# Optimization experiments

Measured on AMD Instinct MI355X. Metric: run time of the kernel, lower is better.

The kernel has to match this reference:

```python
import jax, jax.numpy as jnp
import numpy as np

NEG_SLOPE = 0.01  # nn.LeakyReLU default
NUM_GRAPHS = 64


def leaky_relu(x):
    return jnp.where(x >= 0, x, NEG_SLOPE * x)


def gcn_conv(x, edge_index, W, b):
    """PyG GCNConv: add self-loops, symmetric norm, aggregate, + bias."""
    n = x.shape[0]
    h = x @ W  # [N, F]
    loop = jnp.arange(n, dtype=edge_index.dtype)
    src = jnp.concatenate([edge_index[0], loop])
    dst = jnp.concatenate([edge_index[1], loop])
    deg = jax.ops.segment_sum(jnp.ones_like(dst, dtype=h.dtype), dst, num_segments=n)
    dinv = jnp.where(deg > 0, deg ** -0.5, 0.0)
    norm = dinv[src] * dinv[dst]  # [E+N]
    msg = h[src] * norm[:, None]  # [E+N, F] dominant intermediate
    out = jax.ops.segment_sum(msg, dst, num_segments=n)
    return out + b


def gep(x, batch, num_graphs):
    """global mean pool over batch segment ids."""
    s = jax.ops.segment_sum(x, batch, num_segments=num_graphs)
    cnt = jax.ops.segment_sum(jnp.ones(x.shape[0], dtype=x.dtype), batch, num_segments=num_graphs)
    return s / jnp.maximum(cnt, 1.0)[:, None]


def setup_inputs() -> dict:
    key = jax.random.key(0)
    ks = jax.random.split(key, 16)
    N, E, F, D, B = 10000, 80000, 1024, 128, NUM_GRAPHS
    sc = 1.0 / np.sqrt(F)
    inp = {
        "pro1_x": jax.random.normal(ks[0], (N, F), jnp.float32),
        "pro1_edge_index": jax.random.randint(ks[1], (2, E), 0, N, jnp.int64),
        "pro1_batch": jnp.sort(jax.random.randint(ks[2], (N,), 0, B, jnp.int64)),
        "pro2_x": jax.random.normal(ks[3], (N, F), jnp.float32),
        "pro2_edge_index": jax.random.randint(ks[4], (2, E), 0, N, jnp.int64),
        "pro2_batch": jnp.sort(jax.random.randint(ks[5], (N,), 0, B, jnp.int64)),
        "mas1_straight": 0, "mas1_flipped": 0, "mas2_straight": 0, "mas2_flipped": 0,
        "conv1_W": jax.random.normal(ks[6], (F, F), jnp.float32) * sc,
        "conv1_b": jnp.zeros((F,), jnp.float32),
        "fc1_W": jax.random.normal(ks[7], (F, D), jnp.float32) * sc,
        "fc1_b": jnp.zeros((D,), jnp.float32),
        "conv2_W": jax.random.normal(ks[8], (F, F), jnp.float32) * sc,
        "conv2_b": jnp.zeros((F,), jnp.float32),
        "fc2_W": jax.random.normal(ks[9], (F, D), jnp.float32) * sc,
        "fc2_b": jnp.zeros((D,), jnp.float32),
        "final_W": jax.random.normal(ks[10], (2 * D, 1), jnp.float32) * (1.0 / np.sqrt(2 * D)),
        "final_b": jnp.zeros((1,), jnp.float32),
    }
    return inp


def reference(pro1_x, pro1_edge_index, pro1_batch, pro2_x, pro2_edge_index, pro2_batch,
              mas1_straight, mas1_flipped, mas2_straight, mas2_flipped,
              conv1_W, conv1_b, fc1_W, fc1_b, conv2_W, conv2_b, fc2_W, fc2_b,
              final_W, final_b):
    # branch 1 (dropout = identity at inference)
    x = leaky_relu(gcn_conv(pro1_x, pro1_edge_index, conv1_W, conv1_b))
    x = gep(x, pro1_batch, NUM_GRAPHS)
    x = leaky_relu(x @ fc1_W + fc1_b)
    # branch 2
    xt = leaky_relu(gcn_conv(pro2_x, pro2_edge_index, conv2_W, conv2_b))
    xt = gep(xt, pro2_batch, NUM_GRAPHS)
    xt = leaky_relu(xt @ fc2_W + fc2_b)
    combined = jnp.concatenate([x, xt], axis=1)  # [B, 256]
    return combined @ final_W + final_b  # [B, 1]
```

## Files before the change

### kernel.cpp

```cpp
#include <hip/hip_runtime.h>
#include <cstdint>
#include <cstddef>

#define FDIM 1024
#define DDIM 128
#define NGRAPH 64
#define FCH 8
#define QN 4
#define FILLB 320

#define AS1 __attribute__((address_space(1)))
#define AS3 __attribute__((address_space(3)))

typedef float f32x4 __attribute__((ext_vector_type(4)));
typedef short s16x8 __attribute__((ext_vector_type(8)));
typedef unsigned short u16x8 __attribute__((ext_vector_type(8)));

__device__ __forceinline__ unsigned short f2bf(float f) {
  unsigned int x = __float_as_uint(f);
  unsigned int r = (x + 0x7fffu + ((x >> 16) & 1u)) >> 16;
  return (unsigned short)r;
}
__device__ __forceinline__ float bflo(unsigned int v) {
  return __uint_as_float(v << 16);
}
__device__ __forceinline__ float bfhi(unsigned int v) {
  return __uint_as_float(v & 0xffff0000u);
}

__device__ __forceinline__ int lower_bound(const int* a, int n, int v) {
  int lo = 0, hi = n;
  while (lo < hi) {
    int mid = (lo + hi) >> 1;
    if (a[mid] < v) lo = mid + 1; else hi = mid;
  }
  return lo;
}

__global__ __launch_bounds__(256) void k_prep_cast(const int* __restrict__ ei1,
                                                   const int* __restrict__ ei2,
                                                   int* deg1, int* deg2,
                                                   const float4* __restrict__ x1,
                                                   const float4* __restrict__ x2,
                                                   const float* __restrict__ W1,
                                                   const float* __restrict__ W2,
                                                   u16x8* xb1, u16x8* xb2,
                                                   unsigned short* Wt1, unsigned short* Wt2,
                                                   int E, int n8, int gE, int nxb4) {
  __shared__ unsigned short tile[64][65];
  int br = blockIdx.y;
  int x = blockIdx.x, t = threadIdx.x;
  if (x < gE) {
    const int* ei = br ? ei2 : ei1;
    int* deg = br ? deg2 : deg1;
    int i = x * 256 + t;
    if (i < E) atomicAdd(&deg[ei[E + i]], 1);
  } else if (x < gE + nxb4) {
    const float4* xx = br ? x2 : x1;
    u16x8* xb = br ? xb2 : xb1;
    int base = (x - gE) * 1024 + t;
    #pragma unroll
    for (int u = 0; u < 4; ++u) {
      int i = base + u * 256;
      if (i < n8) {
        float4 v0 = xx[2 * i];
        float4 v1 = xx[2 * i + 1];
        u16x8 o;
        o[0] = f2bf(v0.x); o[1] = f2bf(v0.y); o[2] = f2bf(v0.z); o[3] = f2bf(v0.w);
        o[4] = f2bf(v1.x); o[5] = f2bf(v1.y); o[6] = f2bf(v1.z); o[7] = f2bf(v1.w);
        xb[i] = o;
      }
    }
  } else {
    const float* W = br ? W2 : W1;
    unsigned short* Wt = br ? Wt2 : Wt1;
    int tid16 = x - gE - nxb4;
    int kb = tid16 >> 4, nb = tid16 & 15;
    int tn = t & 63, tg = t >> 6;
    #pragma unroll
    for (int r = 0; r < 16; ++r) {
      int kk = tg * 16 + r;
      tile[kk][tn] = f2bf(W[(size_t)(kb * 64 + kk) * FDIM + nb * 64 + tn]);
    }
    __syncthreads();
    #pragma unroll
    for (int r = 0; r < 16; ++r) {
      int nn = tg * 16 + r;
      Wt[(size_t)(nb * 64 + nn) * FDIM + kb * 64 + tn] = tile[tn][nn];
    }
  }
}

#define SCAN_T 1024
#define SCAN_PER 16
__global__ __launch_bounds__(SCAN_T) void k_scan(const int* __restrict__ deg1,
                                                 const int* __restrict__ deg2,
                                                 int* off1, int* off2,
                                                 int* cur1, int* cur2,
                                                 float* dinv1, float* dinv2,
                                                 const int* __restrict__ batch1,
                                                 const int* __restrict__ batch2,
                                                 int* cnt1, int* gstart1,
                                                 int* cnt2, int* gstart2, int n) {
  if (blockIdx.x == 2) {
    int t = threadIdx.x;
    if (t < 128) {
      const int* batch = (t < NGRAPH) ? batch1 : batch2;
      int* cnt = (t < NGRAPH) ? cnt1 : cnt2;
      int* gstart = (t < NGRAPH) ? gstart1 : gstart2;
      int g = t & (NGRAPH - 1);
      int lo = lower_bound(batch, n, g);
      int hi = lower_bound(batch, n, g + 1);
      gstart[g] = lo;
      cnt[g] = hi - lo;
    }
    return;
  }
  const int* deg = blockIdx.x ? deg2 : deg1;
  int* off = blockIdx.x ? off2 : off1;
  int* cur = blockIdx.x ? cur2 : cur1;
  float* dinv = blockIdx.x ? dinv2 : dinv1;
  __shared__ int sums[SCAN_T];
  int t = threadIdx.x;
  int base = t * SCAN_PER;
  int local[SCAN_PER];
  int s = 0;
  #pragma unroll
  for (int i = 0; i < SCAN_PER; ++i) {
    int idx = base + i;
    int d = (idx < n) ? (deg[idx] + 1) : 0;
    local[i] = s;
    s += d;
    if (idx < n) dinv[idx] = rsqrtf((float)d);
  }
  sums[t] = s;
  __syncthreads();
  for (int o = 1; o < SCAN_T; o <<= 1) {
    int v = (t >= o) ? sums[t - o] : 0;
    __syncthreads();
    sums[t] += v;
    __syncthreads();
  }
  int basesum = (t > 0) ? sums[t - 1] : 0;
  #pragma unroll
  for (int i = 0; i < SCAN_PER; ++i) {
    int idx = base + i;
    if (idx < n) { int o = basesum + local[i]; off[idx] = o; cur[idx] = o; }
  }
  if (t == SCAN_T - 1) off[n] = sums[SCAN_T - 1];
}

__global__ __launch_bounds__(256, 3) void k_fill_gemm(const int* __restrict__ ei1,
                                                      const int* __restrict__ ei2,
                                                      int* cur1, int* cur2,
                                                      const float* __restrict__ dinv1,
                                                      const float* __restrict__ dinv2,
                                                      int* adjsrc1, int* adjsrc2,
                                                      float* adjw1, float* adjw2,
                                                      const unsigned short* __restrict__ A1,
                                                      const unsigned short* __restrict__ A2,
                                                      const unsigned short* __restrict__ B1,
                                                      const unsigned short* __restrict__ B2,
                                                      unsigned short* __restrict__ C1,
                                                      unsigned short* __restrict__ C2,
                                                      int E, int N, int M) {
  __shared__ unsigned short sm[24576];
  int br = blockIdx.y;
  if (blockIdx.x < FILLB) {
    const int* ei = br ? ei2 : ei1;
    int* cur = br ? cur2 : cur1;
    const float* dinv = br ? dinv2 : dinv1;
    int* adjsrc = br ? adjsrc2 : adjsrc1;
    float* adjw = br ? adjw2 : adjw1;
    int i = blockIdx.x * 256 + threadIdx.x;
    if (i < E) {
      int s = ei[i];
      int d = ei[E + i];
      int p = atomicAdd(&cur[d], 1);
      adjsrc[p] = s;
      adjw[p] = dinv[s] * dinv[d];
    }
    if (i < N) {
      int p = atomicAdd(&cur[i], 1);
      adjsrc[p] = i;
      adjw[p] = dinv[i] * dinv[i];
    }
    return;
  }
  const unsigned short* A = br ? A2 : A1;
  const unsigned short* Bt = br ? B2 : B1;
  unsigned short* C = br ? C2 : C1;
  const int K = FDIM;
  int tid = threadIdx.x;
  int w = tid >> 6, lane = tid & 63;
  int wm = w >> 1, wn = w & 1;

  int bx = blockIdx.x - FILLB;
  int per_xcd = (gridDim.x - FILLB) >> 3;
  int l = (bx & 7) * per_xcd + (bx >> 3);
  int m0 = (l >> 3) * 128;
  int n0 = (l & 7) * 128;

  int la = lane & 15, u4 = lane >> 4;

  int rs = w * 32 + (lane >> 2);
  int c16 = (lane & 3) ^ ((lane >> 3) & 3);
  const unsigned short* gA0 = A + (size_t)min(m0 + rs, M - 1) * K + c16 * 8;
  const unsigned short* gA1 = A + (size_t)min(m0 + rs + 16, M - 1) * K + c16 * 8;
  const unsigned short* gB0 = Bt + (size_t)(n0 + rs) * K + c16 * 8;
  const unsigned short* gB1 = Bt + (size_t)(n0 + rs + 16) * K + c16 * 8;
  int lbA = w * 1024;

  int sw = ((la >> 1) & 3) ^ u4;
  unsigned raoff = (unsigned)((wm * 64 + la) * 32 + sw * 8);
  unsigned rboff = (unsigned)(4096 + (wn * 64 + la) * 32 + sw * 8);

  f32x4 acc[4][4];
  #pragma unroll
  for (int i = 0; i < 4; ++i)
    #pragma unroll
    for (int j = 0; j < 4; ++j)
      acc[i][j] = (f32x4){0.f, 0.f, 0.f, 0.f};

  auto STAGE = [&](int bb, int kc) {
    int kq = kc * 32;
    int b0 = bb * 8192 + lbA;
    __builtin_amdgcn_global_load_lds((const AS1 unsigned int*)(gA0 + kq),
                                     (AS3 unsigned int*)&sm[b0], 16, 0, 0);
    __builtin_amdgcn_global_load_lds((const AS1 unsigned int*)(gA1 + kq),
                                     (AS3 unsigned int*)&sm[b0 + 512], 16, 0, 0);
    __builtin_amdgcn_global_load_lds((const AS1 unsigned int*)(gB0 + kq),
                                     (AS3 unsigned int*)&sm[b0 + 4096], 16, 0, 0);
    __builtin_amdgcn_global_load_lds((const AS1 unsigned int*)(gB1 + kq),
                                     (AS3 unsigned int*)&sm[b0 + 4096 + 512], 16, 0, 0);
  };

  auto COMPUTE = [&](int bb) {
    const AS3 unsigned short* pa = (const AS3 unsigned short*)&sm[0] + bb * 8192 + raoff;
    const AS3 unsigned short* pb = (const AS3 unsigned short*)&sm[0] + bb * 8192 + rboff;
    s16x8 a0, a1, a2, a3, b0, b1, b2, b3;
    asm volatile("ds_read_b128 %0, %1 offset:0"    : "=v"(a0) : "v"(pa));
    asm volatile("ds_read_b128 %0, %1 offset:1024" : "=v"(a1) : "v"(pa));
    asm volatile("ds_read_b128 %0, %1 offset:2048" : "=v"(a2) : "v"(pa));
    asm volatile("ds_read_b128 %0, %1 offset:3072" : "=v"(a3) : "v"(pa));
    asm volatile("ds_read_b128 %0, %1 offset:0"    : "=v"(b0) : "v"(pb));
    asm volatile("ds_read_b128 %0, %1 offset:1024" : "=v"(b1) : "v"(pb));
    asm volatile("ds_read_b128 %0, %1 offset:2048" : "=v"(b2) : "v"(pb));
    asm volatile("ds_read_b128 %0, %1 offset:3072" : "=v"(b3) : "v"(pb));
    asm volatile("s_waitcnt lgkmcnt(0)" ::: "memory");
    __builtin_amdgcn_sched_barrier(0);
    __builtin_amdgcn_s_setprio(1);
    acc[0][0] = __builtin_amdgcn_mfma_f32_16x16x32_bf16(a0, b0, acc[0][0], 0, 0, 0);
    acc[0][1] = __builtin_amdgcn_mfma_f32_16x16x32_bf16(a0, b1, acc[0][1], 0, 0, 0);
    acc[0][2] = __builtin_amdgcn_mfma_f32_16x16x32_bf16(a0, b2, acc[0][2], 0, 0, 0);
    acc[0][3] = __builtin_amdgcn_mfma_f32_16x16x32_bf16(a0, b3, acc[0][3], 0, 0, 0);
    acc[1][0] = __builtin_amdgcn_mfma_f32_16x16x32_bf16(a1, b0, acc[1][0], 0, 0, 0);
    acc[1][1] = __builtin_amdgcn_mfma_f32_16x16x32_bf16(a1, b1, acc[1][1], 0, 0, 0);
    acc[1][2] = __builtin_amdgcn_mfma_f32_16x16x32_bf16(a1, b2, acc[1][2], 0, 0, 0);
    acc[1][3] = __builtin_amdgcn_mfma_f32_16x16x32_bf16(a1, b3, acc[1][3], 0, 0, 0);
    acc[2][0] = __builtin_amdgcn_mfma_f32_16x16x32_bf16(a2, b0, acc[2][0], 0, 0, 0);
    acc[2][1] = __builtin_amdgcn_mfma_f32_16x16x32_bf16(a2, b1, acc[2][1], 0, 0, 0);
    acc[2][2] = __builtin_amdgcn_mfma_f32_16x16x32_bf16(a2, b2, acc[2][2], 0, 0, 0);
    acc[2][3] = __builtin_amdgcn_mfma_f32_16x16x32_bf16(a2, b3, acc[2][3], 0, 0, 0);
    acc[3][0] = __builtin_amdgcn_mfma_f32_16x16x32_bf16(a3, b0, acc[3][0], 0, 0, 0);
    acc[3][1] = __builtin_amdgcn_mfma_f32_16x16x32_bf16(a3, b1, acc[3][1], 0, 0, 0);
    acc[3][2] = __builtin_amdgcn_mfma_f32_16x16x32_bf16(a3, b2, acc[3][2], 0, 0, 0);
    acc[3][3] = __builtin_amdgcn_mfma_f32_16x16x32_bf16(a3, b3, acc[3][3], 0, 0, 0);
    __builtin_amdgcn_s_setprio(0);
  };

  STAGE(0, 0);
  STAGE(1, 1);
  int sb = 2, cb = 0;
  for (int kt = 0; kt < 30; ++kt) {
    STAGE(sb, kt + 2);
    asm volatile("s_waitcnt vmcnt(8)" ::: "memory");
    __builtin_amdgcn_sched_barrier(0);
    __builtin_amdgcn_s_barrier();
    COMPUTE(cb);
    __builtin_amdgcn_s_barrier();
    sb = (sb == 2) ? 0 : sb + 1;
    cb = (cb == 2) ? 0 : cb + 1;
  }
  asm volatile("s_waitcnt vmcnt(4)" ::: "memory");
  __builtin_amdgcn_sched_barrier(0);
  __builtin_amdgcn_s_barrier();
  COMPUTE(cb);
  __builtin_amdgcn_s_barrier();
  cb = (cb == 2) ? 0 : cb + 1;
  asm volatile("s_waitcnt vmcnt(0)" ::: "memory");
  __builtin_amdgcn_sched_barrier(0);
  __builtin_amdgcn_s_barrier();
  COMPUTE(cb);

  #pragma unroll
  for (int i = 0; i < 4; ++i) {
    int row_base = m0 + wm * 64 + i * 16 + (lane >> 4) * 4;
    #pragma unroll
    for (int j = 0; j < 4; ++j) {
      int col = n0 + wn * 64 + j * 16 + (lane & 15);
      #pragma unroll
      for (int r = 0; r < 4; ++r) {
        int row = row_base + r;
        if (row < M) C[(size_t)row * FDIM + col] = f2bf(acc[i][j][r]);
      }
    }
  }
}

__global__ __launch_bounds__(256) void k_aggpool(const unsigned short* __restrict__ h1,
                                                 const unsigned short* __restrict__ h2,
                                                 const int* __restrict__ off1,
                                                 const int* __restrict__ off2,
                                                 const int* __restrict__ adjsrc1,
                                                 const int* __restrict__ adjsrc2,
                                                 const float* __restrict__ adjw1,
                                                 const float* __restrict__ adjw2,
                                                 const float* __restrict__ bias1,
                                                 const float* __restrict__ bias2,
                                                 const int* __restrict__ cnt1,
                                                 const int* __restrict__ cnt2,
                                                 const int* __restrict__ gstart1,
                                                 const int* __restrict__ gstart2,
                                                 float* pool4_1, float* pool4_2) {
  int br = blockIdx.y;
  const unsigned short* h = br ? h2 : h1;
  const int* off = br ? off2 : off1;
  const int* adjsrc = br ? adjsrc2 : adjsrc1;
  const float* adjw = br ? adjw2 : adjw1;
  const float* bias = br ? bias2 : bias1;
  const int* cnt = br ? cnt2 : cnt1;
  const int* gstart = br ? gstart2 : gstart1;
  float* pool4 = br ? pool4_2 : pool4_1;

  int x = blockIdx.x;
  int chunk = x & (FCH - 1);
  int r = x >> 3;
  int g = r & (NGRAPH - 1);
  int q = r >> 6;

  int t = threadIdx.x;
  int grp = t >> 6, lane = t & 63;

  int n = cnt[g];
  int start = gstart[g];
  int per = (n + QN - 1) / QN;
  int v0 = start + q * per;
  int v1 = min(start + n, v0 + per);

  int colbase = chunk * 128 + lane * 2;
  const unsigned short* hc = h + colbase;
  float2 b2 = *(const float2*)(bias + colbase);
  float s0 = 0.f, s1 = 0.f;

  for (int v = v0 + grp; v < v1; v += 4) {
    int pb = off[v], pe = off[v + 1];
    float a0 = 0.f, a1 = 0.f;
    for (int pbb = pb; pbb < pe; pbb += 64) {
      int m = min(64, pe - pbb);
      int lp = pbb + ((lane < m) ? lane : (m - 1));
      int vs = adjsrc[lp];
      float vw = adjw[lp];
      int j = 0;
      for (; j + 4 <= m; j += 4) {
        int i0 = __shfl(vs, j),     i1 = __shfl(vs, j + 1);
        int i2 = __shfl(vs, j + 2), i3 = __shfl(vs, j + 3);
        float w0 = __shfl(vw, j),     w1 = __shfl(vw, j + 1);
        float w2 = __shfl(vw, j + 2), w3 = __shfl(vw, j + 3);
        unsigned int h0 = *(const unsigned int*)(hc + ((size_t)i0 << 10));
        unsigned int hv1 = *(const unsigned int*)(hc + ((size_t)i1 << 10));
        unsigned int hv2 = *(const unsigned int*)(hc + ((size_t)i2 << 10));
        unsigned int hv3 = *(const unsigned int*)(hc + ((size_t)i3 << 10));
        a0 += w0 * bflo(h0);  a1 += w0 * bfhi(h0);
        a0 += w1 * bflo(hv1); a1 += w1 * bfhi(hv1);
        a0 += w2 * bflo(hv2); a1 += w2 * bfhi(hv2);
        a0 += w3 * bflo(hv3); a1 += w3 * bfhi(hv3);
      }
      for (; j < m; ++j) {
        int i0 = __shfl(vs, j);
        float w0 = __shfl(vw, j);
        unsigned int h0 = *(const unsigned int*)(hc + ((size_t)i0 << 10));
        a0 += w0 * bflo(h0);
        a1 += w0 * bfhi(h0);
      }
    }
    a0 += b2.x; a1 += b2.y;
    s0 += (a0 >= 0.f) ? a0 : 0.01f * a0;
    s1 += (a1 >= 0.f) ? a1 : 0.01f * a1;
  }

  __shared__ float sm[4][128];
  sm[grp][lane * 2] = s0;
  sm[grp][lane * 2 + 1] = s1;
  __syncthreads();
  if (t < 128) {
    float sum = sm[0][t] + sm[1][t] + sm[2][t] + sm[3][t];
    float ic = 1.0f / fmaxf((float)n, 1.0f);
    pool4[((size_t)(q * NGRAPH + g)) * FDIM + chunk * 128 + t] = sum * ic;
  }
}

__global__ __launch_bounds__(256) void k_fc_final(const float* __restrict__ pool4_1,
                                                  const float* __restrict__ pool4_2,
                                                  const float* __restrict__ W1,
                                                  const float* __restrict__ W2,
                                                  const float* __restrict__ b1,
                                                  const float* __restrict__ b2,
                                                  const float* __restrict__ fW,
                                                  const float* __restrict__ fb,
                                                  float* __restrict__ out) {
  int g = blockIdx.x;
  int t = threadIdx.x;
  int half = t >> 7;
  int j = t & 127;
  const float* pool4 = half ? pool4_2 : pool4_1;
  const float* W = half ? W2 : W1;
  const float* b = half ? b2 : b1;
  __shared__ float xs[2][FDIM];
  for (int k = j; k < FDIM; k += DDIM) {
    float v = 0.f;
    #pragma unroll
    for (int q = 0; q < QN; ++q)
      v += pool4[((size_t)(q * NGRAPH + g)) * FDIM + k];
    xs[half][k] = v;
  }
  __syncthreads();
  float a0 = b[j], a1 = 0.f, a2 = 0.f, a3 = 0.f;
  for (int k = 0; k < FDIM; k += 4) {
    a0 += xs[half][k]     * W[(size_t)k * DDIM + j];
    a1 += xs[half][k + 1] * W[(size_t)(k + 1) * DDIM + j];
    a2 += xs[half][k + 2] * W[(size_t)(k + 2) * DDIM + j];
    a3 += xs[half][k + 3] * W[(size_t)(k + 3) * DDIM + j];
  }
  float acc = (a0 + a1) + (a2 + a3);
  acc = (acc >= 0.f) ? acc : 0.01f * acc;
  float c = acc * fW[half * DDIM + j];
  #pragma unroll
  for (int o = 32; o > 0; o >>= 1) c += __shfl_down(c, o);
  __shared__ float ws[4];
  if ((t & 63) == 0) ws[t >> 6] = c;
  __syncthreads();
  if (t == 0) out[g] = ws[0] + ws[1] + ws[2] + ws[3] + fb[0];
}

extern "C" void kernel_launch(void* const* d_in, const int* in_sizes, int n_in,
                              void* d_out, int out_size, void* d_ws, size_t ws_size,
                              hipStream_t stream) {
  const float* x1 = (const float*)d_in[0];
  const int* ei1 = (const int*)d_in[1];
  const int* batch1 = (const int*)d_in[2];
  const float* x2 = (const float*)d_in[3];
  const int* ei2 = (const int*)d_in[4];
  const int* batch2 = (const int*)d_in[5];
  const float* conv1_W = (const float*)d_in[10];
  const float* conv1_b = (const float*)d_in[11];
  const float* fc1_W = (const float*)d_in[12];
  const float* fc1_b = (const float*)d_in[13];
  const float* conv2_W = (const float*)d_in[14];
  const float* conv2_b = (const float*)d_in[15];
  const float* fc2_W = (const float*)d_in[16];
  const float* fc2_b = (const float*)d_in[17];
  const float* final_W = (const float*)d_in[18];
  const float* final_b = (const float*)d_in[19];
  float* out = (float*)d_out;

  const int N = in_sizes[2];
  const int E = in_sizes[1] / 2;
  const int A = E + N;

  size_t off_b = 0;
  auto alloc = [&](size_t bytes) -> void* {
    void* p = (char*)d_ws + off_b;
    off_b += (bytes + 255) & ~(size_t)255;
    return p;
  };
  unsigned short* xbf1 = (unsigned short*)alloc((size_t)N * FDIM * 2);
  unsigned short* xbf2 = (unsigned short*)alloc((size_t)N * FDIM * 2);
  unsigned short* hbf1 = (unsigned short*)alloc((size_t)N * FDIM * 2);
  unsigned short* hbf2 = (unsigned short*)alloc((size_t)N * FDIM * 2);
  unsigned short* Wt1 = (unsigned short*)alloc((size_t)FDIM * FDIM * 2);
  unsigned short* Wt2 = (unsigned short*)alloc((size_t)FDIM * FDIM * 2);
  int* deg1 = (int*)alloc(N * 4);
  int* deg2 = (int*)alloc(N * 4);
  int* cnt1 = (int*)alloc(NGRAPH * 4);
  int* cnt2 = (int*)alloc(NGRAPH * 4);
  int* gstart1 = (int*)alloc(NGRAPH * 4);
  int* gstart2 = (int*)alloc(NGRAPH * 4);
  int* off1 = (int*)alloc((N + 1) * 4);
  int* off2 = (int*)alloc((N + 1) * 4);
  int* cur1 = (int*)alloc(N * 4);
  int* cur2 = (int*)alloc(N * 4);
  float* dinv1 = (float*)alloc(N * 4);
  float* dinv2 = (float*)alloc(N * 4);
  int* adjsrc1 = (int*)alloc((size_t)A * 4);
  int* adjsrc2 = (int*)alloc((size_t)A * 4);
  float* adjw1 = (float*)alloc((size_t)A * 4);
  float* adjw2 = (float*)alloc((size_t)A * 4);
  float* pool4_1 = (float*)alloc((size_t)QN * NGRAPH * FDIM * 4);
  float* pool4_2 = (float*)alloc((size_t)QN * NGRAPH * FDIM * 4);

  const int T = 256;
  int gE = (E + T - 1) / T;
  int n8 = N * FDIM / 8;
  int nxb4 = (n8 + 1023) / 1024;
  int mt = (N + 127) / 128;
  dim3 gPrepCast(gE + nxb4 + 256, 2);
  dim3 gFillGemm(FILLB + mt * 8, 2);
  dim3 gAgg(FCH * NGRAPH * QN, 2);

  size_t degspan = (size_t)((char*)deg2 - (char*)deg1) + (size_t)N * 4;
  hipMemsetAsync(deg1, 0, degspan, stream);
  k_prep_cast<<<gPrepCast, T, 0, stream>>>(ei1, ei2, deg1, deg2,
                                           (const float4*)x1, (const float4*)x2,
                                           conv1_W, conv2_W,
                                           (u16x8*)xbf1, (u16x8*)xbf2, Wt1, Wt2,
                                           E, n8, gE, nxb4);
  k_scan<<<3, SCAN_T, 0, stream>>>(deg1, deg2, off1, off2, cur1, cur2, dinv1, dinv2,
                                   batch1, batch2, cnt1, gstart1, cnt2, gstart2, N);
  k_fill_gemm<<<gFillGemm, T, 0, stream>>>(ei1, ei2, cur1, cur2, dinv1, dinv2,
                                           adjsrc1, adjsrc2, adjw1, adjw2,
                                           xbf1, xbf2, Wt1, Wt2, hbf1, hbf2,
                                           E, N, N);
  k_aggpool<<<gAgg, T, 0, stream>>>(hbf1, hbf2, off1, off2, adjsrc1, adjsrc2,
                                    adjw1, adjw2, conv1_b, conv2_b,
                                    cnt1, cnt2, gstart1, gstart2, pool4_1, pool4_2);
  k_fc_final<<<NGRAPH, T, 0, stream>>>(pool4_1, pool4_2, fc1_W, fc2_W, fc1_b, fc2_b,
                                       final_W, final_b, out);
}
```

Baseline: 318.3 us.

## Process two K-tiles per barrier pair with four-buffer LDS ping-pong in GEMM

```diff
diff --git a/kernel.cpp b/kernel.cpp
--- a/kernel.cpp
+++ b/kernel.cpp
@@ -150,7 +150,7 @@
   if (t == SCAN_T - 1) off[n] = sums[SCAN_T - 1];
 }
 
-__global__ __launch_bounds__(256, 3) void k_fill_gemm(const int* __restrict__ ei1,
+__global__ __launch_bounds__(256, 2) void k_fill_gemm(const int* __restrict__ ei1,
                                                       const int* __restrict__ ei2,
                                                       int* cur1, int* cur2,
                                                       const float* __restrict__ dinv1,
@@ -164,7 +164,7 @@
                                                       unsigned short* __restrict__ C1,
                                                       unsigned short* __restrict__ C2,
                                                       int E, int N, int M) {
-  __shared__ unsigned short sm[24576];
+  __shared__ unsigned short sm[32768];
   int br = blockIdx.y;
   if (blockIdx.x < FILLB) {
     const int* ei = br ? ei2 : ei1;
@@ -235,63 +235,76 @@
                                      (AS3 unsigned int*)&sm[b0 + 4096 + 512], 16, 0, 0);
   };
 
-  auto COMPUTE = [&](int bb) {
-    const AS3 unsigned short* pa = (const AS3 unsigned short*)&sm[0] + bb * 8192 + raoff;
-    const AS3 unsigned short* pb = (const AS3 unsigned short*)&sm[0] + bb * 8192 + rboff;
-    s16x8 a0, a1, a2, a3, b0, b1, b2, b3;
-    asm volatile("ds_read_b128 %0, %1 offset:0"    : "=v"(a0) : "v"(pa));
-    asm volatile("ds_read_b128 %0, %1 offset:1024" : "=v"(a1) : "v"(pa));
-    asm volatile("ds_read_b128 %0, %1 offset:2048" : "=v"(a2) : "v"(pa));
-    asm volatile("ds_read_b128 %0, %1 offset:3072" : "=v"(a3) : "v"(pa));
-    asm volatile("ds_read_b128 %0, %1 offset:0"    : "=v"(b0) : "v"(pb));
-    asm volatile("ds_read_b128 %0, %1 offset:1024" : "=v"(b1) : "v"(pb));
-    asm volatile("ds_read_b128 %0, %1 offset:2048" : "=v"(b2) : "v"(pb));
-    asm volatile("ds_read_b128 %0, %1 offset:3072" : "=v"(b3) : "v"(pb));
+  #define MFMA16(aa, bb)                                                            \
+    acc[0][0] = __builtin_amdgcn_mfma_f32_16x16x32_bf16(aa[0], bb[0], acc[0][0], 0, 0, 0); \
+    acc[0][1] = __builtin_amdgcn_mfma_f32_16x16x32_bf16(aa[0], bb[1], acc[0][1], 0, 0, 0); \
+    acc[0][2] = __builtin_amdgcn_mfma_f32_16x16x32_bf16(aa[0], bb[2], acc[0][2], 0, 0, 0); \
+    acc[0][3] = __builtin_amdgcn_mfma_f32_16x16x32_bf16(aa[0], bb[3], acc[0][3], 0, 0, 0); \
+    acc[1][0] = __builtin_amdgcn_mfma_f32_16x16x32_bf16(aa[1], bb[0], acc[1][0], 0, 0, 0); \
+    acc[1][1] = __builtin_amdgcn_mfma_f32_16x16x32_bf16(aa[1], bb[1], acc[1][1], 0, 0, 0); \
+    acc[1][2] = __builtin_amdgcn_mfma_f32_16x16x32_bf16(aa[1], bb[2], acc[1][2], 0, 0, 0); \
+    acc[1][3] = __builtin_amdgcn_mfma_f32_16x16x32_bf16(aa[1], bb[3], acc[1][3], 0, 0, 0); \
+    acc[2][0] = __builtin_amdgcn_mfma_f32_16x16x32_bf16(aa[2], bb[0], acc[2][0], 0, 0, 0); \
+    acc[2][1] = __builtin_amdgcn_mfma_f32_16x16x32_bf16(aa[2], bb[1], acc[2][1], 0, 0, 0); \
+    acc[2][2] = __builtin_amdgcn_mfma_f32_16x16x32_bf16(aa[2], bb[2], acc[2][2], 0, 0, 0); \
+    acc[2][3] = __builtin_amdgcn_mfma_f32_16x16x32_bf16(aa[2], bb[3], acc[2][3], 0, 0, 0); \
+    acc[3][0] = __builtin_amdgcn_mfma_f32_16x16x32_bf16(aa[3], bb[0], acc[3][0], 0, 0, 0); \
+    acc[3][1] = __builtin_amdgcn_mfma_f32_16x16x32_bf16(aa[3], bb[1], acc[3][1], 0, 0, 0); \
+    acc[3][2] = __builtin_amdgcn_mfma_f32_16x16x32_bf16(aa[3], bb[2], acc[3][2], 0, 0, 0); \
+    acc[3][3] = __builtin_amdgcn_mfma_f32_16x16x32_bf16(aa[3], bb[3], acc[3][3], 0, 0, 0);
+
+  auto COMPUTE_PAIR = [&](int b0i, int b1i) {
+    const AS3 unsigned short* base = (const AS3 unsigned short*)&sm[0];
+    const AS3 unsigned short* pa0 = base + b0i * 8192 + raoff;
+    const AS3 unsigned short* pb0 = base + b0i * 8192 + rboff;
+    const AS3 unsigned short* pa1 = base + b1i * 8192 + raoff;
+    const AS3 unsigned short* pb1 = base + b1i * 8192 + rboff;
+    s16x8 a0[4], b0v[4], a1[4], b1v[4];
+    asm volatile("ds_read_b128 %0, %1 offset:0"    : "=v"(a0[0]) : "v"(pa0));
+    asm volatile("ds_read_b128 %0, %1 offset:1024" : "=v"(a0[1]) : "v"(pa0));
+    asm volatile("ds_read_b128 %0, %1 offset:2048" : "=v"(a0[2]) : "v"(pa0));
+    asm volatile("ds_read_b128 %0, %1 offset:3072" : "=v"(a0[3]) : "v"(pa0));
+    asm volatile("ds_read_b128 %0, %1 offset:0"    : "=v"(b0v[0]) : "v"(pb0));
+    asm volatile("ds_read_b128 %0, %1 offset:1024" : "=v"(b0v[1]) : "v"(pb0));
+    asm volatile("ds_read_b128 %0, %1 offset:2048" : "=v"(b0v[2]) : "v"(pb0));
+    asm volatile("ds_read_b128 %0, %1 offset:3072" : "=v"(b0v[3]) : "v"(pb0));
+    asm volatile("ds_read_b128 %0, %1 offset:0"    : "=v"(a1[0]) : "v"(pa1));
+    asm volatile("ds_read_b128 %0, %1 offset:1024" : "=v"(a1[1]) : "v"(pa1));
+    asm volatile("ds_read_b128 %0, %1 offset:2048" : "=v"(a1[2]) : "v"(pa1));
+    asm volatile("ds_read_b128 %0, %1 offset:3072" : "=v"(a1[3]) : "v"(pa1));
+    asm volatile("ds_read_b128 %0, %1 offset:0"    : "=v"(b1v[0]) : "v"(pb1));
+    asm volatile("ds_read_b128 %0, %1 offset:1024" : "=v"(b1v[1]) : "v"(pb1));
+    asm volatile("ds_read_b128 %0, %1 offset:2048" : "=v"(b1v[2]) : "v"(pb1));
+    asm volatile("ds_read_b128 %0, %1 offset:3072" : "=v"(b1v[3]) : "v"(pb1));
+    asm volatile("s_waitcnt lgkmcnt(8)" ::: "memory");
+    __builtin_amdgcn_sched_barrier(0);
+    __builtin_amdgcn_s_setprio(1);
+    MFMA16(a0, b0v)
+    __builtin_amdgcn_s_setprio(0);
     asm volatile("s_waitcnt lgkmcnt(0)" ::: "memory");
     __builtin_amdgcn_sched_barrier(0);
     __builtin_amdgcn_s_setprio(1);
-    acc[0][0] = __builtin_amdgcn_mfma_f32_16x16x32_bf16(a0, b0, acc[0][0], 0, 0, 0);
-    acc[0][1] = __builtin_amdgcn_mfma_f32_16x16x32_bf16(a0, b1, acc[0][1], 0, 0, 0);
-    acc[0][2] = __builtin_amdgcn_mfma_f32_16x16x32_bf16(a0, b2, acc[0][2], 0, 0, 0);
-    acc[0][3] = __builtin_amdgcn_mfma_f32_16x16x32_bf16(a0, b3, acc[0][3], 0, 0, 0);
-    acc[1][0] = __builtin_amdgcn_mfma_f32_16x16x32_bf16(a1, b0, acc[1][0], 0, 0, 0);
-    acc[1][1] = __builtin_amdgcn_mfma_f32_16x16x32_bf16(a1, b1, acc[1][1], 0, 0, 0);
-    acc[1][2] = __builtin_amdgcn_mfma_f32_16x16x32_bf16(a1, b2, acc[1][2], 0, 0, 0);
-    acc[1][3] = __builtin_amdgcn_mfma_f32_16x16x32_bf16(a1, b3, acc[1][3], 0, 0, 0);
-    acc[2][0] = __builtin_amdgcn_mfma_f32_16x16x32_bf16(a2, b0, acc[2][0], 0, 0, 0);
-    acc[2][1] = __builtin_amdgcn_mfma_f32_16x16x32_bf16(a2, b1, acc[2][1], 0, 0, 0);
-    acc[2][2] = __builtin_amdgcn_mfma_f32_16x16x32_bf16(a2, b2, acc[2][2], 0, 0, 0);
-    acc[2][3] = __builtin_amdgcn_mfma_f32_16x16x32_bf16(a2, b3, acc[2][3], 0, 0, 0);
-    acc[3][0] = __builtin_amdgcn_mfma_f32_16x16x32_bf16(a3, b0, acc[3][0], 0, 0, 0);
-    acc[3][1] = __builtin_amdgcn_mfma_f32_16x16x32_bf16(a3, b1, acc[3][1], 0, 0, 0);
-    acc[3][2] = __builtin_amdgcn_mfma_f32_16x16x32_bf16(a3, b2, acc[3][2], 0, 0, 0);
-    acc[3][3] = __builtin_amdgcn_mfma_f32_16x16x32_bf16(a3, b3, acc[3][3], 0, 0, 0);
+    MFMA16(a1, b1v)
     __builtin_amdgcn_s_setprio(0);
   };
 
   STAGE(0, 0);
   STAGE(1, 1);
-  int sb = 2, cb = 0;
-  for (int kt = 0; kt < 30; ++kt) {
-    STAGE(sb, kt + 2);
+  for (int s = 0; s < 15; ++s) {
+    int pb = ((s + 1) & 1) * 2;
+    STAGE(pb, 2 * s + 2);
+    STAGE(pb + 1, 2 * s + 3);
     asm volatile("s_waitcnt vmcnt(8)" ::: "memory");
     __builtin_amdgcn_sched_barrier(0);
     __builtin_amdgcn_s_barrier();
-    COMPUTE(cb);
+    int cbp = (s & 1) * 2;
+    COMPUTE_PAIR(cbp, cbp + 1);
     __builtin_amdgcn_s_barrier();
-    sb = (sb == 2) ? 0 : sb + 1;
-    cb = (cb == 2) ? 0 : cb + 1;
-  }
-  asm volatile("s_waitcnt vmcnt(4)" ::: "memory");
-  __builtin_amdgcn_sched_barrier(0);
-  __builtin_amdgcn_s_barrier();
-  COMPUTE(cb);
-  __builtin_amdgcn_s_barrier();
-  cb = (cb == 2) ? 0 : cb + 1;
+  }
   asm volatile("s_waitcnt vmcnt(0)" ::: "memory");
   __builtin_amdgcn_sched_barrier(0);
   __builtin_amdgcn_s_barrier();
-  COMPUTE(cb);
+  COMPUTE_PAIR(2, 3);
 
   #pragma unroll
   for (int i = 0; i < 4; ++i) {
@@ -306,6 +319,7 @@
       }
     }
   }
+  #undef MFMA16
 }
 
 __global__ __launch_bounds__(256) void k_aggpool(const unsigned short* __restrict__ h1,
```

Result: no change. 322.2 us, median of 2 (+1.2%).
